# Kernel optimization log

Hardware: AMD Instinct MI355X
Metric: run time of the kernel (lower is better)

The kernel has to match this reference:

```python
import jax, jax.numpy as jnp
import numpy as np

K = 3
KK = K * K
PAD = 1          # kernel_size // 2
MAX_SHIFT = 8.0  # bias_range > 0
DEG = 2          # degrees = (2, 2), paon_type 'a'


def setup_inputs() -> dict:
    key = jax.random.key(0)
    ks = jax.random.split(key, 6)
    B, C, O, H, W = 4, 64, 64, 160, 160
    x = jax.random.normal(ks[0], (B, C, H, W), jnp.float32)
    # offset conv is 1x1: weight [2*K*K, C], bias [2*K*K]
    off_w = jax.random.normal(ks[1], (2 * KK, C), jnp.float32) * 0.1
    off_b = jax.random.normal(ks[2], (2 * KK,), jnp.float32) * 0.1
    scale = 1.0 / np.sqrt(C * KK).astype(np.float32)
    w_m = jax.random.normal(ks[3], (DEG * O, C, K, K), jnp.float32) * scale
    w_n = jax.random.normal(ks[4], (DEG * O, C, K, K), jnp.float32) * scale
    w0 = jax.random.normal(ks[5], (O,), jnp.float32) * 0.1
    return {"x": x, "off_w": off_w, "off_b": off_b, "w_m": w_m, "w_n": w_n, "w0": w0}


def _bilinear_sample(x, py, px):
    """x: [B,C,H,W]; py,px: [B,KK,H,W] -> [B,C,KK,H,W]; zero outside bounds."""
    B, C, H, W = x.shape
    xf = x.reshape(B, C, H * W)
    y0 = jnp.floor(py)
    x0 = jnp.floor(px)
    wy = py - y0
    wx = px - x0
    y0i = y0.astype(jnp.int32)
    x0i = x0.astype(jnp.int32)
    out = jnp.zeros((B, C) + py.shape[1:], x.dtype)
    corners = ((0, 0, (1 - wy) * (1 - wx)), (0, 1, (1 - wy) * wx),
               (1, 0, wy * (1 - wx)), (1, 1, wy * wx))
    for dy, dx, wgt in corners:
        yy = y0i + dy
        xx = x0i + dx
        valid = (yy >= 0) & (yy < H) & (xx >= 0) & (xx < W)
        idx = jnp.clip(yy, 0, H - 1) * W + jnp.clip(xx, 0, W - 1)
        g = jax.vmap(lambda f, i: f[:, i])(xf, idx.reshape(B, -1))  # [B,C,KK*H*W]
        out = out + g.reshape(B, C, *py.shape[1:]) * (wgt * valid)[:, None]
    return out


def _after_poly_a(y, ch, o, take_abs):
    # channel reorder + groupwise sum, per PaLaBase.after_poly_a
    order = np.array([(k * ch) % (ch * o) + k // o for k in range(ch * o)])
    y = y[:, order].reshape(y.shape[0], ch, o, *y.shape[2:])
    return jnp.abs(y).sum(2) if take_abs else y.sum(2)


def reference(x, off_w, off_b, w_m, w_n, w0):
    B, C, H, W = x.shape
    O = w0.shape[0]
    # --- DeformOffset: 1x1 conv -> clamp to image -> tanh soft-limit ---
    off_r = jnp.einsum('bchw,oc->bohw', x, off_w) + off_b[None, :, None, None]
    gy = jnp.arange(H, dtype=x.dtype)[None, None, :, None]
    gx = jnp.arange(W, dtype=x.dtype)[None, None, None, :]
    oy = jnp.clip(off_r[:, 0::2], -gy, H - gy)  # [B,KK,H,W] (dy per kernel pos)
    ox = jnp.clip(off_r[:, 1::2], -gx, W - gx)  # [B,KK,H,W] (dx per kernel pos)
    soft = lambda o: jnp.where(jnp.abs(o) >= MAX_SHIFT,
                               MAX_SHIFT * jnp.tanh(o / MAX_SHIFT), o)
    oy, ox = soft(oy), soft(ox)
    # --- deformable sampling grid (stride=1, dilation=1, zero padding) ---
    kidx = jnp.arange(KK)
    kh = (kidx // K).astype(x.dtype)[None, :, None, None]
    kw = (kidx % K).astype(x.dtype)[None, :, None, None]
    base_y = (jnp.arange(H, dtype=x.dtype) - PAD)[None, None, :, None]
    base_x = (jnp.arange(W, dtype=x.dtype) - PAD)[None, None, None, :]
    py = base_y + kh + oy
    px = base_x + kw + ox
    samp = _bilinear_sample(x, py, px)  # [B,C,KK,H,W]
    # --- Pade numerator / denominator convs on the sampled tensor ---
    pm_raw = jnp.einsum('bckhw,ock->bohw', samp, w_m.reshape(DEG * O, C, KK))
    qn_raw = jnp.einsum('bckhw,ock->bohw', samp, w_n.reshape(DEG * O, C, KK))
    pm = _after_poly_a(pm_raw, O, DEG, take_abs=False)
    qn = _after_poly_a(qn_raw, O, DEG, take_abs=True)
    # prepare_for_div_a: (pm + w0, 1 + qn)
    return (pm + w0[None, :, None, None]) / (1.0 + qn)
```

## Files before the change

### kernel.cpp

```cpp
#include <hip/hip_runtime.h>

#define Hh 160
#define Ww 160
#define Cc 64
#define HWc 25600
#define Bb 4

typedef __attribute__((ext_vector_type(8))) short short8;
typedef __attribute__((ext_vector_type(4))) float f32x4;

__device__ __forceinline__ unsigned short f2bf(float f) {
  unsigned int u = __float_as_uint(f);
  unsigned int r = u + 0x7FFFu + ((u >> 16) & 1u);
  return (unsigned short)(r >> 16);
}
__device__ __forceinline__ float bflo(unsigned int u) {
  return __uint_as_float(u << 16);
}
__device__ __forceinline__ float bfhi(unsigned int u) {
  return __uint_as_float(u & 0xffff0000u);
}

__global__ __launch_bounds__(256) void k_transpose(const float* __restrict__ x,
                                                   unsigned short* __restrict__ xT) {
  __shared__ unsigned short s[64][65];
  int wg = blockIdx.x;
  int b = wg / 400;
  int pix0 = (wg % 400) * 64;
  int l = threadIdx.x & 63, wv = threadIdx.x >> 6;
  const float* xb = x + (size_t)b * Cc * HWc + pix0;
#pragma unroll
  for (int i = 0; i < 16; i++) {
    int c = i * 4 + wv;
    s[c][l] = f2bf(xb[(size_t)c * HWc + l]);
  }
  __syncthreads();
  int p = threadIdx.x >> 2, ck = threadIdx.x & 3;
  unsigned int w[8];
#pragma unroll
  for (int j = 0; j < 8; j++) {
    unsigned int a = s[ck * 16 + 2 * j][p];
    unsigned int bb = s[ck * 16 + 2 * j + 1][p];
    w[j] = a | (bb << 16);
  }
  unsigned short* dst = xT + ((size_t)(b * HWc + pix0 + p)) * 64 + ck * 16;
  ((uint4*)dst)[0] = make_uint4(w[0], w[1], w[2], w[3]);
  ((uint4*)dst)[1] = make_uint4(w[4], w[5], w[6], w[7]);
}

__global__ __launch_bounds__(256) void k_wpack(const float* __restrict__ wm,
                                               const float* __restrict__ wn,
                                               const float* __restrict__ ow,
                                               unsigned short* __restrict__ bf) {
  int i = blockIdx.x * 256 + threadIdx.x;
  if (i < 9 * 2 * 12 * 64 * 8) {
    int j2 = i & 7;
    int lane = (i >> 3) & 63;
    int ntck = i >> 9;
    int nt = ntck % 12;
    int ck = ntck / 12;
    int kk = ck >> 1;
    int chunk = ck & 1;
    int n = nt * 16 + (lane & 15);
    int c = chunk * 32 + (lane >> 4) * 8 + j2;
    float v;
    if (n < 64)
      v = wm[(n * 64 + c) * 9 + kk] + wm[((n + 64) * 64 + c) * 9 + kk];
    else
      v = wn[((n - 64) * 64 + c) * 9 + kk];
    bf[i] = f2bf(v);
  } else if (i < 9 * 2 * 12 * 64 * 8 + 2 * 2 * 64 * 8) {
    int j = i - 9 * 2 * 12 * 64 * 8;
    int j2 = j & 7;
    int lane = (j >> 3) & 63;
    int rest = j >> 9;
    int ntile = rest & 1;
    int chunk = rest >> 1;
    int n = ntile * 16 + (lane & 15);
    int c = chunk * 32 + (lane >> 4) * 8 + j2;
    bf[i] = (n < 18) ? f2bf(ow[n * 64 + c]) : (unsigned short)0;
  }
}

__device__ __forceinline__ void gather_batch(
    const unsigned short* __restrict__ xTb, float2 P, int ch8, uint4& c00,
    uint4& c01, uint4& c10, uint4& c11, float& w00, float& w01, float& w10,
    float& w11) {
  float py = P.x, pxv = P.y;
  float y0f = floorf(py), x0f = floorf(pxv);
  float wy = py - y0f, wx = pxv - x0f;
  int y0 = (int)y0f, x0 = (int)x0f;
  float vy0 = (y0 >= 0 && y0 < Hh) ? 1.f : 0.f;
  float vy1 = (y0 >= -1 && y0 < Hh - 1) ? 1.f : 0.f;
  float vx0 = (x0 >= 0 && x0 < Ww) ? 1.f : 0.f;
  float vx1 = (x0 >= -1 && x0 < Ww - 1) ? 1.f : 0.f;
  int r0 = min(max(y0, 0), Hh - 1) * Ww;
  int r1 = min(max(y0 + 1, 0), Hh - 1) * Ww;
  int c0 = min(max(x0, 0), Ww - 1);
  int c1 = min(max(x0 + 1, 0), Ww - 1);
  w00 = (1.f - wy) * (1.f - wx) * vy0 * vx0;
  w01 = (1.f - wy) * wx * vy0 * vx1;
  w10 = wy * (1.f - wx) * vy1 * vx0;
  w11 = wy * wx * vy1 * vx1;
  const unsigned short* g = xTb + ch8 * 8;
  c00 = *(const uint4*)(g + (size_t)(r0 + c0) * 64);
  c01 = *(const uint4*)(g + (size_t)(r0 + c1) * 64);
  c10 = *(const uint4*)(g + (size_t)(r1 + c0) * 64);
  c11 = *(const uint4*)(g + (size_t)(r1 + c1) * 64);
}

__device__ __forceinline__ void combine_write(unsigned short* Arow,
                                              const uint4& c00, const uint4& c01,
                                              const uint4& c10, const uint4& c11,
                                              float w00, float w01, float w10,
                                              float w11) {
  const unsigned int* a = (const unsigned int*)&c00;
  const unsigned int* b = (const unsigned int*)&c01;
  const unsigned int* c = (const unsigned int*)&c10;
  const unsigned int* d = (const unsigned int*)&c11;
  unsigned int o[4];
#pragma unroll
  for (int j = 0; j < 4; j++) {
    float lo = bflo(a[j]) * w00 + bflo(b[j]) * w01 + bflo(c[j]) * w10 +
               bflo(d[j]) * w11;
    float hi = bfhi(a[j]) * w00 + bfhi(b[j]) * w01 + bfhi(c[j]) * w10 +
               bfhi(d[j]) * w11;
    o[j] = (unsigned int)f2bf(lo) | ((unsigned int)f2bf(hi) << 16);
  }
  *(uint4*)Arow = make_uint4(o[0], o[1], o[2], o[3]);
}

__global__ __launch_bounds__(256) void k_main(
    const unsigned short* __restrict__ xT, const float* __restrict__ w0,
    const float* __restrict__ off_b, const unsigned short* __restrict__ bfrag,
    const unsigned short* __restrict__ obfrag, float* __restrict__ out) {
  __shared__ unsigned short A[2][64 * 72];
  __shared__ float2 spybuf[9][64];
  const int tid = threadIdx.x;
  const int wg = blockIdx.x;
  const int band = wg & 7;
  const int local = wg >> 3;
  const int b = local / 50;
  const int pix0 = band * 3200 + (local % 50) * 64;
  const int wv = tid >> 6;
  const int l = tid & 63;
  const int lm = l & 15;
  const int quad = l >> 4;
  const int ch8 = l & 7;
  const int pr = l >> 3;

  const unsigned short* xTb = xT + (size_t)b * HWc * 64;

  f32x4 acc[3][4];
  const f32x4 zero = {0.f, 0.f, 0.f, 0.f};
#pragma unroll
  for (int j = 0; j < 3; j++)
#pragma unroll
    for (int pt = 0; pt < 4; pt++) acc[j][pt] = zero;

  {
    f32x4 aO0 = zero, aO1 = zero;
    const unsigned short* xrow = xTb + (size_t)(pix0 + wv * 16 + lm) * 64;
#pragma unroll
    for (int chunk = 0; chunk < 2; chunk++) {
      short8 sb = *(const short8*)(xrow + chunk * 32 + quad * 8);
      short8 wf0 = *(const short8*)&obfrag[((chunk * 2 + 0) * 64 + l) * 8];
      short8 wf1 = *(const short8*)&obfrag[((chunk * 2 + 1) * 64 + l) * 8];
      aO0 = __builtin_amdgcn_mfma_f32_16x16x32_bf16(wf0, sb, aO0, 0, 0, 0);
      aO1 = __builtin_amdgcn_mfma_f32_16x16x32_bf16(wf1, sb, aO1, 0, 0, 0);
    }
    int pix = pix0 + wv * 16 + lm;
    int h = pix / Ww, w = pix % Ww;
    float fh = (float)h, fw = (float)w;
#pragma unroll
    for (int rr = 0; rr < 2; rr++) {
      int n = quad * 4 + 2 * rr;
      int kk = n >> 1;
      float oy = aO0[2 * rr] + off_b[n];
      float ox = aO0[2 * rr + 1] + off_b[n + 1];
      oy = fminf(fmaxf(oy, -fh), 160.0f - fh);
      ox = fminf(fmaxf(ox, -fw), 160.0f - fw);
      if (fabsf(oy) >= 8.0f) oy = 8.0f * tanhf(oy * 0.125f);
      if (fabsf(ox) >= 8.0f) ox = 8.0f * tanhf(ox * 0.125f);
      spybuf[kk][wv * 16 + lm] =
          make_float2(fh - 1.0f + (float)(kk / 3) + oy,
                      fw - 1.0f + (float)(kk % 3) + ox);
    }
    if (quad == 0) {
      float oy = aO1[0] + off_b[16];
      float ox = aO1[1] + off_b[17];
      oy = fminf(fmaxf(oy, -fh), 160.0f - fh);
      ox = fminf(fmaxf(ox, -fw), 160.0f - fw);
      if (fabsf(oy) >= 8.0f) oy = 8.0f * tanhf(oy * 0.125f);
      if (fabsf(ox) >= 8.0f) ox = 8.0f * tanhf(ox * 0.125f);
      spybuf[8][wv * 16 + lm] =
          make_float2(fh - 1.0f + 2.0f + oy, fw - 1.0f + 2.0f + ox);
    }
  }
  __syncthreads();

#pragma unroll
  for (int i = 0; i < 2; i++) {
    int pl = wv * 16 + i * 8 + pr;
    uint4 c00, c01, c10, c11;
    float w00, w01, w10, w11;
    gather_batch(xTb, spybuf[0][pl], ch8, c00, c01, c10, c11, w00, w01, w10,
                 w11);
    combine_write(&A[0][pl * 72 + ch8 * 8], c00, c01, c10, c11, w00, w01, w10,
                  w11);
  }
  __syncthreads();

  for (int kk = 0; kk < 9; kk++) {
    const int cur = kk & 1;
    uint4 g00[2], g01[2], g10[2], g11[2];
    float W00[2], W01[2], W10[2], W11[2];
    if (kk < 8) {
#pragma unroll
      for (int i = 0; i < 2; i++) {
        int pl = wv * 16 + i * 8 + pr;
        gather_batch(xTb, spybuf[kk + 1][pl], ch8, g00[i], g01[i], g10[i],
                     g11[i], W00[i], W01[i], W10[i], W11[i]);
      }
    }
#pragma unroll
    for (int chunk = 0; chunk < 2; chunk++) {
      short8 sfr[4];
#pragma unroll
      for (int pt = 0; pt < 4; pt++)
        sfr[pt] =
            *(const short8*)&A[cur][(pt * 16 + lm) * 72 + chunk * 32 + quad * 8];
      short8 wfr[3];
#pragma unroll
      for (int j = 0; j < 3; j++) {
        int nt = j * 4 + wv;
        wfr[j] = *(const short8*)&bfrag[((size_t)((kk * 2 + chunk) * 12 + nt) *
                                            64 + l) * 8];
      }
#pragma unroll
      for (int j = 0; j < 3; j++)
#pragma unroll
        for (int pt = 0; pt < 4; pt++)
          acc[j][pt] = __builtin_amdgcn_mfma_f32_16x16x32_bf16(
              wfr[j], sfr[pt], acc[j][pt], 0, 0, 0);
    }
    if (kk < 8) {
#pragma unroll
      for (int i = 0; i < 2; i++) {
        int pl = wv * 16 + i * 8 + pr;
        combine_write(&A[cur ^ 1][pl * 72 + ch8 * 8], g00[i], g01[i], g10[i],
                      g11[i], W00[i], W01[i], W10[i], W11[i]);
      }
    }
    __syncthreads();
  }

  float w0v[4];
#pragma unroll
  for (int r = 0; r < 4; r++) w0v[r] = w0[wv * 16 + quad * 4 + r];
  float* ob = out + (size_t)b * Cc * HWc + pix0;
#pragma unroll
  for (int pt = 0; pt < 4; pt++) {
#pragma unroll
    for (int r = 0; r < 4; r++) {
      int oc = wv * 16 + quad * 4 + r;
      float pm = acc[0][pt][r] + w0v[r];
      float qn = 1.0f + fabsf(acc[1][pt][r]) + fabsf(acc[2][pt][r]);
      ob[oc * HWc + pt * 16 + lm] = pm / qn;
    }
  }
}

extern "C" void kernel_launch(void* const* d_in, const int* in_sizes, int n_in,
                              void* d_out, int out_size, void* d_ws, size_t ws_size,
                              hipStream_t stream) {
  const float* x = (const float*)d_in[0];
  const float* off_w = (const float*)d_in[1];
  const float* off_b = (const float*)d_in[2];
  const float* w_m = (const float*)d_in[3];
  const float* w_n = (const float*)d_in[4];
  const float* w0 = (const float*)d_in[5];
  float* out = (float*)d_out;

  unsigned short* bfrag = (unsigned short*)d_ws;
  unsigned short* obfrag = (unsigned short*)((char*)d_ws + (size_t)221184);
  unsigned short* xT = (unsigned short*)((char*)d_ws + (size_t)225280);

  hipLaunchKernelGGL(k_transpose, dim3(1600), dim3(256), 0, stream, x, xT);
  hipLaunchKernelGGL(k_wpack, dim3(440), dim3(256), 0, stream, w_m, w_n, off_w,
                     bfrag);
  hipLaunchKernelGGL(k_main, dim3(1600), dim3(256), 0, stream, xT, w0, off_b,
                     bfrag, obfrag, out);
}
```

Before: 134.5 us.

## Precompute bilinear gather descriptors once per block and merge prep kernels

Each block now computes the bilinear sampling address, neighbor deltas and fp16 corner weights once per (kernel position, pixel) into a shared descriptor table. Previously every channel-group lane recomputed floor, clamp and weights itself, and the table reuses the A buffer for the staging coordinates. The transpose and weight-pack kernels are merged into one launch to save a kernel launch. The bf16 packing also switches to the HIP intrinsic. Storing the corner weights as fp16 adds a little rounding error, and the extra barrier and descriptor pass add some work per block.

```diff
diff --git a/kernel.cpp b/kernel.cpp
--- a/kernel.cpp
+++ b/kernel.cpp
@@ -1,4 +1,6 @@
 #include <hip/hip_runtime.h>
+#include <hip/hip_bf16.h>
+#include <hip/hip_fp16.h>
 
 #define Hh 160
 #define Ww 160
@@ -21,92 +23,80 @@
   return __uint_as_float(u & 0xffff0000u);
 }
 
-__global__ __launch_bounds__(256) void k_transpose(const float* __restrict__ x,
-                                                   unsigned short* __restrict__ xT) {
-  __shared__ unsigned short s[64][65];
-  int wg = blockIdx.x;
-  int b = wg / 400;
-  int pix0 = (wg % 400) * 64;
-  int l = threadIdx.x & 63, wv = threadIdx.x >> 6;
-  const float* xb = x + (size_t)b * Cc * HWc + pix0;
-#pragma unroll
-  for (int i = 0; i < 16; i++) {
-    int c = i * 4 + wv;
-    s[c][l] = f2bf(xb[(size_t)c * HWc + l]);
-  }
-  __syncthreads();
-  int p = threadIdx.x >> 2, ck = threadIdx.x & 3;
-  unsigned int w[8];
-#pragma unroll
-  for (int j = 0; j < 8; j++) {
-    unsigned int a = s[ck * 16 + 2 * j][p];
-    unsigned int bb = s[ck * 16 + 2 * j + 1][p];
-    w[j] = a | (bb << 16);
-  }
-  unsigned short* dst = xT + ((size_t)(b * HWc + pix0 + p)) * 64 + ck * 16;
-  ((uint4*)dst)[0] = make_uint4(w[0], w[1], w[2], w[3]);
-  ((uint4*)dst)[1] = make_uint4(w[4], w[5], w[6], w[7]);
-}
-
-__global__ __launch_bounds__(256) void k_wpack(const float* __restrict__ wm,
-                                               const float* __restrict__ wn,
-                                               const float* __restrict__ ow,
-                                               unsigned short* __restrict__ bf) {
-  int i = blockIdx.x * 256 + threadIdx.x;
-  if (i < 9 * 2 * 12 * 64 * 8) {
-    int j2 = i & 7;
-    int lane = (i >> 3) & 63;
-    int ntck = i >> 9;
-    int nt = ntck % 12;
-    int ck = ntck / 12;
-    int kk = ck >> 1;
-    int chunk = ck & 1;
-    int n = nt * 16 + (lane & 15);
-    int c = chunk * 32 + (lane >> 4) * 8 + j2;
-    float v;
-    if (n < 64)
-      v = wm[(n * 64 + c) * 9 + kk] + wm[((n + 64) * 64 + c) * 9 + kk];
-    else
-      v = wn[((n - 64) * 64 + c) * 9 + kk];
-    bf[i] = f2bf(v);
-  } else if (i < 9 * 2 * 12 * 64 * 8 + 2 * 2 * 64 * 8) {
-    int j = i - 9 * 2 * 12 * 64 * 8;
-    int j2 = j & 7;
-    int lane = (j >> 3) & 63;
-    int rest = j >> 9;
-    int ntile = rest & 1;
-    int chunk = rest >> 1;
-    int n = ntile * 16 + (lane & 15);
-    int c = chunk * 32 + (lane >> 4) * 8 + j2;
-    bf[i] = (n < 18) ? f2bf(ow[n * 64 + c]) : (unsigned short)0;
-  }
-}
-
-__device__ __forceinline__ void gather_batch(
-    const unsigned short* __restrict__ xTb, float2 P, int ch8, uint4& c00,
-    uint4& c01, uint4& c10, uint4& c11, float& w00, float& w01, float& w10,
-    float& w11) {
-  float py = P.x, pxv = P.y;
-  float y0f = floorf(py), x0f = floorf(pxv);
-  float wy = py - y0f, wx = pxv - x0f;
-  int y0 = (int)y0f, x0 = (int)x0f;
-  float vy0 = (y0 >= 0 && y0 < Hh) ? 1.f : 0.f;
-  float vy1 = (y0 >= -1 && y0 < Hh - 1) ? 1.f : 0.f;
-  float vx0 = (x0 >= 0 && x0 < Ww) ? 1.f : 0.f;
-  float vx1 = (x0 >= -1 && x0 < Ww - 1) ? 1.f : 0.f;
-  int r0 = min(max(y0, 0), Hh - 1) * Ww;
-  int r1 = min(max(y0 + 1, 0), Hh - 1) * Ww;
-  int c0 = min(max(x0, 0), Ww - 1);
-  int c1 = min(max(x0 + 1, 0), Ww - 1);
-  w00 = (1.f - wy) * (1.f - wx) * vy0 * vx0;
-  w01 = (1.f - wy) * wx * vy0 * vx1;
-  w10 = wy * (1.f - wx) * vy1 * vx0;
-  w11 = wy * wx * vy1 * vx1;
-  const unsigned short* g = xTb + ch8 * 8;
-  c00 = *(const uint4*)(g + (size_t)(r0 + c0) * 64);
-  c01 = *(const uint4*)(g + (size_t)(r0 + c1) * 64);
-  c10 = *(const uint4*)(g + (size_t)(r1 + c0) * 64);
-  c11 = *(const uint4*)(g + (size_t)(r1 + c1) * 64);
+__global__ __launch_bounds__(256) void k_prep(
+    const float* __restrict__ x, const float* __restrict__ wm,
+    const float* __restrict__ wn, const float* __restrict__ ow,
+    unsigned short* __restrict__ xT, unsigned short* __restrict__ bf) {
+  if (blockIdx.x < 1600) {
+    __shared__ unsigned short s[64][65];
+    int wg = blockIdx.x;
+    int b = wg / 400;
+    int pix0 = (wg % 400) * 64;
+    int l = threadIdx.x & 63, wv = threadIdx.x >> 6;
+    const float* xb = x + (size_t)b * Cc * HWc + pix0;
+#pragma unroll
+    for (int i = 0; i < 16; i++) {
+      int c = i * 4 + wv;
+      s[c][l] = f2bf(xb[(size_t)c * HWc + l]);
+    }
+    __syncthreads();
+    int p = threadIdx.x >> 2, ck = threadIdx.x & 3;
+    unsigned int w[8];
+#pragma unroll
+    for (int j = 0; j < 8; j++) {
+      unsigned int a = s[ck * 16 + 2 * j][p];
+      unsigned int bb = s[ck * 16 + 2 * j + 1][p];
+      w[j] = a | (bb << 16);
+    }
+    unsigned short* dst = xT + ((size_t)(b * HWc + pix0 + p)) * 64 + ck * 16;
+    ((uint4*)dst)[0] = make_uint4(w[0], w[1], w[2], w[3]);
+    ((uint4*)dst)[1] = make_uint4(w[4], w[5], w[6], w[7]);
+  } else {
+    int i = (blockIdx.x - 1600) * 256 + threadIdx.x;
+    if (i < 9 * 2 * 12 * 64 * 8) {
+      int j2 = i & 7;
+      int lane = (i >> 3) & 63;
+      int ntck = i >> 9;
+      int nt = ntck % 12;
+      int ck = ntck / 12;
+      int kk = ck >> 1;
+      int chunk = ck & 1;
+      int n = nt * 16 + (lane & 15);
+      int c = chunk * 32 + (lane >> 4) * 8 + j2;
+      float v;
+      if (n < 64)
+        v = wm[(n * 64 + c) * 9 + kk] + wm[((n + 64) * 64 + c) * 9 + kk];
+      else
+        v = wn[((n - 64) * 64 + c) * 9 + kk];
+      bf[i] = f2bf(v);
+    } else if (i < 9 * 2 * 12 * 64 * 8 + 2 * 2 * 64 * 8) {
+      int j = i - 9 * 2 * 12 * 64 * 8;
+      int j2 = j & 7;
+      int lane = (j >> 3) & 63;
+      int rest = j >> 9;
+      int ntile = rest & 1;
+      int chunk = rest >> 1;
+      int n = ntile * 16 + (lane & 15);
+      int c = chunk * 32 + (lane >> 4) * 8 + j2;
+      bf[i] = (n < 18) ? f2bf(ow[n * 64 + c]) : (unsigned short)0;
+    }
+  }
+}
+
+__device__ __forceinline__ void gather2(const char* __restrict__ gbase, uint4 D,
+                                        int chB, uint4& c00, uint4& c01,
+                                        uint4& c10, uint4& c11, float& w00,
+                                        float& w01, float& w10, float& w11) {
+  int bb = D.x + chB;
+  int dxB = (int)(D.y & 0xffffu);
+  int dyB = (int)(D.y >> 16);
+  c00 = *(const uint4*)(gbase + bb);
+  c01 = *(const uint4*)(gbase + bb + dxB);
+  c10 = *(const uint4*)(gbase + bb + dyB);
+  c11 = *(const uint4*)(gbase + bb + (dxB + dyB));
+  float2 wA = __half22float2(*(const __half2*)&D.z);
+  float2 wB = __half22float2(*(const __half2*)&D.w);
+  w00 = wA.x; w01 = wA.y; w10 = wB.x; w11 = wB.y;
 }
 
 __device__ __forceinline__ void combine_write(unsigned short* Arow,
@@ -125,7 +115,8 @@
                bflo(d[j]) * w11;
     float hi = bfhi(a[j]) * w00 + bfhi(b[j]) * w01 + bfhi(c[j]) * w10 +
                bfhi(d[j]) * w11;
-    o[j] = (unsigned int)f2bf(lo) | ((unsigned int)f2bf(hi) << 16);
+    __hip_bfloat162 hh = __float22bfloat162_rn(make_float2(lo, hi));
+    o[j] = *(unsigned int*)&hh;
   }
   *(uint4*)Arow = make_uint4(o[0], o[1], o[2], o[3]);
 }
@@ -135,7 +126,8 @@
     const float* __restrict__ off_b, const unsigned short* __restrict__ bfrag,
     const unsigned short* __restrict__ obfrag, float* __restrict__ out) {
   __shared__ unsigned short A[2][64 * 72];
-  __shared__ float2 spybuf[9][64];
+  __shared__ uint4 gdesc[576];
+  float2* spy = (float2*)&A[0][0];
   const int tid = threadIdx.x;
   const int wg = blockIdx.x;
   const int band = wg & 7;
@@ -148,8 +140,10 @@
   const int quad = l >> 4;
   const int ch8 = l & 7;
   const int pr = l >> 3;
+  const int chB = ch8 * 16;
 
   const unsigned short* xTb = xT + (size_t)b * HWc * 64;
+  const char* gbase = (const char*)xTb;
 
   f32x4 acc[3][4];
   const f32x4 zero = {0.f, 0.f, 0.f, 0.f};
@@ -182,7 +176,7 @@
       ox = fminf(fmaxf(ox, -fw), 160.0f - fw);
       if (fabsf(oy) >= 8.0f) oy = 8.0f * tanhf(oy * 0.125f);
       if (fabsf(ox) >= 8.0f) ox = 8.0f * tanhf(ox * 0.125f);
-      spybuf[kk][wv * 16 + lm] =
+      spy[kk * 64 + wv * 16 + lm] =
           make_float2(fh - 1.0f + (float)(kk / 3) + oy,
                       fw - 1.0f + (float)(kk % 3) + ox);
     }
@@ -193,9 +187,38 @@
       ox = fminf(fmaxf(ox, -fw), 160.0f - fw);
       if (fabsf(oy) >= 8.0f) oy = 8.0f * tanhf(oy * 0.125f);
       if (fabsf(ox) >= 8.0f) ox = 8.0f * tanhf(ox * 0.125f);
-      spybuf[8][wv * 16 + lm] =
-          make_float2(fh - 1.0f + 2.0f + oy, fw - 1.0f + 2.0f + ox);
-    }
+      spy[8 * 64 + wv * 16 + lm] =
+          make_float2(fh + 1.0f + oy, fw + 1.0f + ox);
+    }
+  }
+  __syncthreads();
+
+  for (int e = tid; e < 576; e += 256) {
+    float2 P = spy[e];
+    float py = P.x, pxv = P.y;
+    float y0f = floorf(py), x0f = floorf(pxv);
+    float wy = py - y0f, wx = pxv - x0f;
+    int y0 = (int)y0f, x0 = (int)x0f;
+    float vy0 = (y0 >= 0 && y0 < Hh) ? 1.f : 0.f;
+    float vy1 = (y0 >= -1 && y0 < Hh - 1) ? 1.f : 0.f;
+    float vx0 = (x0 >= 0 && x0 < Ww) ? 1.f : 0.f;
+    float vx1 = (x0 >= -1 && x0 < Ww - 1) ? 1.f : 0.f;
+    int r0 = min(max(y0, 0), Hh - 1);
+    int r1 = min(max(y0 + 1, 0), Hh - 1);
+    int c0 = min(max(x0, 0), Ww - 1);
+    int c1 = min(max(x0 + 1, 0), Ww - 1);
+    float w00 = (1.f - wy) * (1.f - wx) * vy0 * vx0;
+    float w01 = (1.f - wy) * wx * vy0 * vx1;
+    float w10 = wy * (1.f - wx) * vy1 * vx0;
+    float w11 = wy * wx * vy1 * vx1;
+    uint4 D;
+    D.x = (unsigned int)((r0 * Ww + c0) * 128);
+    D.y = (unsigned int)((c1 - c0) * 128) | ((unsigned int)((r1 - r0) * Ww * 128) << 16);
+    __half2 hA = __floats2half2_rn(w00, w01);
+    __half2 hB = __floats2half2_rn(w10, w11);
+    D.z = *(unsigned int*)&hA;
+    D.w = *(unsigned int*)&hB;
+    gdesc[e] = D;
   }
   __syncthreads();
 
@@ -204,8 +227,7 @@
     int pl = wv * 16 + i * 8 + pr;
     uint4 c00, c01, c10, c11;
     float w00, w01, w10, w11;
-    gather_batch(xTb, spybuf[0][pl], ch8, c00, c01, c10, c11, w00, w01, w10,
-                 w11);
+    gather2(gbase, gdesc[pl], chB, c00, c01, c10, c11, w00, w01, w10, w11);
     combine_write(&A[0][pl * 72 + ch8 * 8], c00, c01, c10, c11, w00, w01, w10,
                   w11);
   }
@@ -219,8 +241,8 @@
 #pragma unroll
       for (int i = 0; i < 2; i++) {
         int pl = wv * 16 + i * 8 + pr;
-        gather_batch(xTb, spybuf[kk + 1][pl], ch8, g00[i], g01[i], g10[i],
-                     g11[i], W00[i], W01[i], W10[i], W11[i]);
+        gather2(gbase, gdesc[(kk + 1) * 64 + pl], chB, g00[i], g01[i], g10[i],
+                g11[i], W00[i], W01[i], W10[i], W11[i]);
       }
     }
 #pragma unroll
@@ -286,9 +308,8 @@
   unsigned short* obfrag = (unsigned short*)((char*)d_ws + (size_t)221184);
   unsigned short* xT = (unsigned short*)((char*)d_ws + (size_t)225280);
 
-  hipLaunchKernelGGL(k_transpose, dim3(1600), dim3(256), 0, stream, x, xT);
-  hipLaunchKernelGGL(k_wpack, dim3(440), dim3(256), 0, stream, w_m, w_n, off_w,
-                     bfrag);
+  hipLaunchKernelGGL(k_prep, dim3(2040), dim3(256), 0, stream, x, w_m, w_n,
+                     off_w, xT, bfrag);
   hipLaunchKernelGGL(k_main, dim3(1600), dim3(256), 0, stream, xT, w0, off_b,
                      bfrag, obfrag, out);
 }
```

Measured after the change: 134.1 us. No clear change (-0.3%).
